# Performance work log

Hardware: AMD Instinct MI355X
Metric: run time of the kernel (lower is better)

## Reference

```python
import jax, jax.numpy as jnp
import numpy as np

E = 256      # feat_dim
H = 4        # num_heads
D = E // H   # head_dim = 64
NC = 7       # num_classes
B = 65536
EPS = 1e-5


def layernorm(x, g, b):
    mu = jnp.mean(x, axis=-1, keepdims=True)
    var = jnp.mean((x - mu) ** 2, axis=-1, keepdims=True)
    return (x - mu) * jax.lax.rsqrt(var + EPS) * g + b


def setup_inputs() -> dict:
    key = jax.random.key(0)
    ks = jax.random.split(key, 16)
    s = 0.02
    return {
        "f_swin":   jax.random.normal(ks[0], (B, E), jnp.float32),
        "f_maxvit": jax.random.normal(ks[1], (B, E), jnp.float32),
        "f_focal":  jax.random.normal(ks[2], (B, E), jnp.float32),
        # MultiheadAttention params (torch packs q,k,v into in_proj)
        "in_proj_w": jax.random.normal(ks[3], (3 * E, E), jnp.float32) * s,
        "in_proj_b": jnp.zeros((3 * E,), jnp.float32),
        "out_w": jax.random.normal(ks[4], (E, E), jnp.float32) * s,
        "out_b": jnp.zeros((E,), jnp.float32),
        # fusion LayerNorm
        "ln1_g": jnp.ones((E,), jnp.float32),
        "ln1_b": jnp.zeros((E,), jnp.float32),
        # gate: Linear(3E, 3)
        "gate_w": jax.random.normal(ks[5], (3, 3 * E), jnp.float32) * s,
        "gate_b": jnp.zeros((3,), jnp.float32),
        # deep_head: LN -> Linear(E,256) -> GELU -> Linear(256,128) -> GELU -> Linear(128,7)
        "ln2_g": jnp.ones((E,), jnp.float32),
        "ln2_b": jnp.zeros((E,), jnp.float32),
        "w1": jax.random.normal(ks[6], (256, E), jnp.float32) * s,
        "b1": jnp.zeros((256,), jnp.float32),
        "w2": jax.random.normal(ks[7], (128, 256), jnp.float32) * s,
        "b2": jnp.zeros((128,), jnp.float32),
        "w3": jax.random.normal(ks[8], (NC, 128), jnp.float32) * s,
        "b3": jnp.zeros((NC,), jnp.float32),
    }


def reference(f_swin, f_maxvit, f_focal, in_proj_w, in_proj_b, out_w, out_b,
              ln1_g, ln1_b, gate_w, gate_b, ln2_g, ln2_b,
              w1, b1, w2, b2, w3, b3):
    # --- AttentionFusionModule ---
    stacked = jnp.stack([f_swin, f_maxvit, f_focal], axis=1)  # [B,3,E]
    qkv = stacked @ in_proj_w.T + in_proj_b                   # [B,3,3E]
    q, k, v = jnp.split(qkv, 3, axis=-1)
    # [B,3,E] -> [B,H,3,D]
    def to_heads(t):
        return t.reshape(t.shape[0], 3, H, D).transpose(0, 2, 1, 3)
    qh, kh, vh = to_heads(q), to_heads(k), to_heads(v)
    scores = jnp.einsum('bhqd,bhkd->bhqk', qh, kh) / jnp.sqrt(jnp.float32(D))
    attn = jax.nn.softmax(scores, axis=-1)
    ctx = jnp.einsum('bhqk,bhkd->bhqd', attn, vh)             # [B,H,3,D]
    ctx = ctx.transpose(0, 2, 1, 3).reshape(-1, 3, E)         # [B,3,E]
    att_out = ctx @ out_w.T + out_b
    x = layernorm(att_out + stacked, ln1_g, ln1_b)            # [B,3,E]
    concat = jnp.concatenate([f_swin, f_maxvit, f_focal], axis=-1)  # [B,3E]
    weights = jax.nn.softmax(concat @ gate_w.T + gate_b, axis=-1)   # [B,3]
    fused = jnp.einsum('bse,bs->be', x, weights)              # [B,E]
    # --- deep_head (Dropout inactive at inference; exact GELU as in torch) ---
    h = layernorm(fused, ln2_g, ln2_b)
    h = jax.nn.gelu(h @ w1.T + b1, approximate=False)
    h = jax.nn.gelu(h @ w2.T + b2, approximate=False)
    logits = h @ w3.T + b3
    return logits, fused
```

## Files before the change

kernel.cpp:

```cpp
#include <hip/hip_runtime.h>
#include <math.h>


#define E   256
#define NC  7
#define BM  16
#define TOK 48
#define NT  256
#define BS  264

typedef unsigned short u16;
typedef unsigned int   u32;
typedef __attribute__((ext_vector_type(8))) short  short8;
typedef __attribute__((ext_vector_type(4))) float  f32x4;

#define O_IPW 0
#define O_OW  196608
#define O_GW  262144
#define O_W1  264448
#define O_W2  329984
#define CVT_TOTAL 362752

__device__ __forceinline__ float bf2f(u32 u) { return __uint_as_float(u << 16); }
__device__ __forceinline__ u16 f2bf(float f) {
    u32 u = __float_as_uint(f);
    return (u16)((u + 0x7fffu + ((u >> 16) & 1u)) >> 16);
}

__global__ void cvt_weights(const float* __restrict__ ipw, const float* __restrict__ ow,
                            const float* __restrict__ gw,  const float* __restrict__ w1,
                            const float* __restrict__ w2,  u16* __restrict__ ws) {
    int i4 = (blockIdx.x * 256 + threadIdx.x) * 4;
    if (i4 >= CVT_TOTAL) return;
    const float* src; int off;
    if      (i4 < O_OW)  { src = ipw; off = i4; }
    else if (i4 < O_GW)  { src = ow;  off = i4 - O_OW; }
    else if (i4 < O_W1)  { src = gw;  off = i4 - O_GW; }
    else if (i4 < O_W2)  { src = w1;  off = i4 - O_W1; }
    else                 { src = w2;  off = i4 - O_W2; }
    float4 v = *(const float4*)(src + off);
    ushort4 o;
    o.x = f2bf(v.x); o.y = f2bf(v.y); o.z = f2bf(v.z); o.w = f2bf(v.w);
    *(ushort4*)(ws + i4) = o;
}

template<int NTW>
__device__ __forceinline__ void issue_b(const u16* __restrict__ bW, int rowBase, int lane,
                                        short8 (&b)[8][NTW]) {
    const int l16 = lane & 15, quad = lane >> 4;
    #pragma unroll
    for (int ks = 0; ks < 8; ++ks)
        #pragma unroll
        for (int j = 0; j < NTW; ++j)
            b[ks][j] = *(const short8*)(bW + (size_t)(rowBase + j * 16 + l16) * 256 + ks * 32 + quad * 8);
}

template<int MT, int NTW>
__device__ __forceinline__ void consume_gemm(const u16* aLds, int aRow0, int lane,
                                             const short8 (&b)[8][NTW], f32x4 (&acc)[MT][NTW]) {
    const int l16 = lane & 15, quad = lane >> 4;
    #pragma unroll
    for (int m = 0; m < MT; ++m)
        #pragma unroll
        for (int j = 0; j < NTW; ++j) acc[m][j] = (f32x4){0.f, 0.f, 0.f, 0.f};
    #pragma unroll
    for (int ks = 0; ks < 8; ++ks) {
        short8 a[MT];
        #pragma unroll
        for (int m = 0; m < MT; ++m)
            a[m] = *(const short8*)(aLds + (size_t)(aRow0 + m * 16 + l16) * BS + ks * 32 + quad * 8);
        #pragma unroll
        for (int j = 0; j < NTW; ++j)
            #pragma unroll
            for (int m = 0; m < MT; ++m)
                acc[m][j] = __builtin_amdgcn_mfma_f32_16x16x32_bf16(a[m], b[ks][j], acc[m][j], 0, 0, 0);
    }
}

__global__ __launch_bounds__(NT, 2)
void dhc_mfma_kernel(
    const float* __restrict__ f0, const float* __restrict__ f1, const float* __restrict__ f2,
    const float* __restrict__ ipb, const float* __restrict__ ob,
    const float* __restrict__ ln1g, const float* __restrict__ ln1b,
    const float* __restrict__ gb,
    const float* __restrict__ ln2g, const float* __restrict__ ln2b,
    const float* __restrict__ b1, const float* __restrict__ b2,
    const float* __restrict__ w3, const float* __restrict__ b3,
    const u16* __restrict__ ws, float* __restrict__ d_out, int nrows)
{
    __shared__ __align__(16) u16 s_x[TOK * BS];
    __shared__ __align__(16) u16 s_buf[TOK * BS];
    __shared__ __align__(16) float s_small[576];
    #define S_ATTN(r,h,q) s_small[((r) * 4 + (h)) * 9 + (q)]
    float* s_mu    = s_small;
    float* s_rstd  = s_small + 48;
    float* s_mu2   = s_small + 96;
    float* s_rstd2 = s_small + 112;

    const int tid  = threadIdx.x;
    const int wid  = tid >> 6, lane = tid & 63;
    const int l16  = lane & 15, quad = lane >> 4;
    const long long row0 = (long long)blockIdx.x * BM;
    const size_t fused_base = (size_t)nrows * NC;

    auto pad_slot = [&](int i) -> float* {
        return (float*)(s_buf + (i >> 2) * BS + 256) + (i & 3);
    };

    const u16* ipw_b = ws + O_IPW;
    const u16* ow_b  = ws + O_OW;
    const u16* gw_b  = ws + O_GW;
    const u16* w1_b  = ws + O_W1;
    const u16* w2_b  = ws + O_W2;

    short8 bq[8][4];
    short8 b5[8][2];

    const int rb0 = (wid < 2) ? (64 * wid) : (256 + 64 * (wid - 2));
    issue_b<4>(ipw_b, rb0, lane, bq);

    #pragma unroll
    for (int it = 0; it < 12; ++it) {
        int id = it * NT + tid;
        int t  = id >> 6;
        int c4 = (id & 63) * 4;
        int s  = t >> 4, r = t & 15;
        float4 v = {0.f, 0.f, 0.f, 0.f};
        if (row0 + r < nrows) {
            const float* src = (s == 0 ? f0 : (s == 1 ? f1 : f2));
            v = *(const float4*)(src + (size_t)(row0 + r) * E + c4);
        }
        ushort4 o;
        o.x = f2bf(v.x); o.y = f2bf(v.y); o.z = f2bf(v.z); o.w = f2bf(v.w);
        *(ushort4*)(s_x + t * BS + c4) = o;
    }
    __syncthreads();

    for (int p = 0; p < 2; ++p) {
        const int rb = rb0 + 128 * p;
        f32x4 acc[3][4];
        consume_gemm<3, 4>(s_x, 0, lane, bq, acc);
        issue_b<4>(ipw_b, (p == 0) ? (rb0 + 128) : (512 + 64 * wid), lane, bq);
        #pragma unroll
        for (int j = 0; j < 4; ++j) {
            int n = wid * 64 + j * 16 + l16;
            float bias = ipb[rb + j * 16 + l16];
            #pragma unroll
            for (int m = 0; m < 3; ++m)
                #pragma unroll
                for (int rr = 0; rr < 4; ++rr) {
                    int tok = m * 16 + quad * 4 + rr;
                    s_buf[tok * BS + n] = f2bf(acc[m][j][rr] + bias);
                }
        }
        __syncthreads();
        if (tid < 96) {
            int r = tid / 6, rem = tid % 6;
            int hh = rem / 3, i = rem % 3;
            int h = 2 * p + hh;
            float d0a = 0.f, d0b = 0.f, d1a = 0.f, d1b = 0.f, d2a = 0.f, d2b = 0.f;
            const u16* qrow = s_buf + (i * 16 + r) * BS + hh * 64;
            const u16* k0 = s_buf + (0 * 16 + r) * BS + 128 + hh * 64;
            const u16* k1 = s_buf + (1 * 16 + r) * BS + 128 + hh * 64;
            const u16* k2 = s_buf + (2 * 16 + r) * BS + 128 + hh * 64;
            for (int d8 = 0; d8 < 8; ++d8) {
                short8 qv = *(const short8*)(qrow + d8 * 8);
                short8 a0 = *(const short8*)(k0 + d8 * 8);
                short8 a1 = *(const short8*)(k1 + d8 * 8);
                short8 a2 = *(const short8*)(k2 + d8 * 8);
                #pragma unroll
                for (int e = 0; e < 4; ++e) {
                    float qa = bf2f((u32)(u16)qv[e]);
                    float qb = bf2f((u32)(u16)qv[e + 4]);
                    d0a += qa * bf2f((u32)(u16)a0[e]); d0b += qb * bf2f((u32)(u16)a0[e + 4]);
                    d1a += qa * bf2f((u32)(u16)a1[e]); d1b += qb * bf2f((u32)(u16)a1[e + 4]);
                    d2a += qa * bf2f((u32)(u16)a2[e]); d2b += qb * bf2f((u32)(u16)a2[e + 4]);
                }
            }
            float d0 = (d0a + d0b) * 0.125f, d1 = (d1a + d1b) * 0.125f, d2 = (d2a + d2b) * 0.125f;
            float mx = fmaxf(d0, fmaxf(d1, d2));
            float e0 = __expf(d0 - mx), e1 = __expf(d1 - mx), e2 = __expf(d2 - mx);
            float inv = 1.f / (e0 + e1 + e2);
            S_ATTN(r, h, i * 3 + 0) = e0 * inv;
            S_ATTN(r, h, i * 3 + 1) = e1 * inv;
            S_ATTN(r, h, i * 3 + 2) = e2 * inv;
        } else if (p == 0 && tid < 240) {
            int idx = tid - 96;
            int r = idx / 9, rem = idx % 9;
            int g = rem / 3, s = rem % 3;
            const u16* xp = s_x + (s * 16 + r) * BS;
            const u16* wp = gw_b + g * 768 + s * 256;
            float a0 = 0.f, a1 = 0.f, a2 = 0.f, a3 = 0.f;
            for (int c8 = 0; c8 < 8; ++c8) {
                #pragma unroll
                for (int q4 = 0; q4 < 4; ++q4) {
                    short8 xv = *(const short8*)(xp + (c8 * 4 + q4) * 8);
                    short8 wv = *(const short8*)(wp + (c8 * 4 + q4) * 8);
                    float t = 0.f;
                    #pragma unroll
                    for (int e = 0; e < 8; ++e)
                        t += bf2f((u32)(u16)xv[e]) * bf2f((u32)(u16)wv[e]);
                    if      (q4 == 0) a0 += t;
                    else if (q4 == 1) a1 += t;
                    else if (q4 == 2) a2 += t;
                    else              a3 += t;
                }
            }
            *pad_slot(idx) = (a0 + a1) + (a2 + a3);
        } else if (p == 1 && tid < 112) {
            int r = tid - 96;
            float l[3];
            #pragma unroll
            for (int g = 0; g < 3; ++g)
                l[g] = gb[g] + *pad_slot(r * 9 + g * 3 + 0)
                             + *pad_slot(r * 9 + g * 3 + 1)
                             + *pad_slot(r * 9 + g * 3 + 2);
            float mx = fmaxf(l[0], fmaxf(l[1], l[2]));
            float e0 = __expf(l[0] - mx), e1 = __expf(l[1] - mx), e2 = __expf(l[2] - mx);
            float inv = 1.f / (e0 + e1 + e2);
            *pad_slot(144 + r * 3 + 0) = e0 * inv;
            *pad_slot(144 + r * 3 + 1) = e1 * inv;
            *pad_slot(144 + r * 3 + 2) = e2 * inv;
        }
        __syncthreads();
    }

    {
        const int rb = 512 + 64 * wid;
        f32x4 acc[3][4];
        consume_gemm<3, 4>(s_x, 0, lane, bq, acc);
        issue_b<4>(ow_b, 64 * wid, lane, bq);
        #pragma unroll
        for (int j = 0; j < 4; ++j) {
            int n = wid * 64 + j * 16 + l16;
            float bias = ipb[rb + j * 16 + l16];
            #pragma unroll
            for (int m = 0; m < 3; ++m)
                #pragma unroll
                for (int rr = 0; rr < 4; ++rr) {
                    int tok = m * 16 + quad * 4 + rr;
                    s_buf[tok * BS + n] = f2bf(acc[m][j][rr] + bias);
                }
        }
    }
    __syncthreads();

    {
        int r = tid >> 4;
        int cb = (tid & 15) * 16;
        int h = cb >> 6;
        float a[9];
        #pragma unroll
        for (int q2 = 0; q2 < 9; ++q2) a[q2] = S_ATTN(r, h, q2);
        #pragma unroll
        for (int cc = 0; cc < 16; ++cc) {
            int c = cb + cc;
            float v0 = bf2f((u32)s_buf[(0 * 16 + r) * BS + c]);
            float v1 = bf2f((u32)s_buf[(1 * 16 + r) * BS + c]);
            float v2 = bf2f((u32)s_buf[(2 * 16 + r) * BS + c]);
            float c0 = a[0] * v0 + a[1] * v1 + a[2] * v2;
            float c1 = a[3] * v0 + a[4] * v1 + a[5] * v2;
            float c2 = a[6] * v0 + a[7] * v1 + a[8] * v2;
            s_buf[(0 * 16 + r) * BS + c] = f2bf(c0);
            s_buf[(1 * 16 + r) * BS + c] = f2bf(c1);
            s_buf[(2 * 16 + r) * BS + c] = f2bf(c2);
        }
    }
    __syncthreads();

    {
        const int rb = 64 * wid;
        f32x4 acc[3][4];
        consume_gemm<3, 4>(s_buf, 0, lane, bq, acc);
        issue_b<4>(w1_b, 64 * wid, lane, bq);
        #pragma unroll
        for (int j = 0; j < 4; ++j) {
            int n = rb + j * 16 + l16;
            float bias = ob[n];
            #pragma unroll
            for (int m = 0; m < 3; ++m)
                #pragma unroll
                for (int rr = 0; rr < 4; ++rr) {
                    int tok = m * 16 + quad * 4 + rr;
                    acc[m][j][rr] += bias + bf2f((u32)s_x[tok * BS + n]);
                }
        }
        __syncthreads();
        #pragma unroll
        for (int j = 0; j < 4; ++j) {
            int n = rb + j * 16 + l16;
            #pragma unroll
            for (int m = 0; m < 3; ++m)
                #pragma unroll
                for (int rr = 0; rr < 4; ++rr) {
                    int tok = m * 16 + quad * 4 + rr;
                    s_buf[tok * BS + n] = f2bf(acc[m][j][rr]);
                }
        }
    }
    __syncthreads();

    if (tid < 192) {
        int r = tid >> 2, j = tid & 3;
        const u16* xp = s_buf + r * BS + j * 64;
        float s0 = 0.f, s1 = 0.f, q0 = 0.f, q1 = 0.f;
        #pragma unroll
        for (int c8 = 0; c8 < 8; ++c8) {
            short8 v = *(const short8*)(xp + c8 * 8);
            #pragma unroll
            for (int e = 0; e < 4; ++e) {
                float xa = bf2f((u32)(u16)v[e]);
                float xb = bf2f((u32)(u16)v[e + 4]);
                s0 += xa; q0 += xa * xa;
                s1 += xb; q1 += xb * xb;
            }
        }
        float sum = s0 + s1, sq = q0 + q1;
        sum += __shfl_xor(sum, 1); sq += __shfl_xor(sq, 1);
        sum += __shfl_xor(sum, 2); sq += __shfl_xor(sq, 2);
        if (j == 0) {
            float mu = sum * (1.f / 256.f);
            float var = sq * (1.f / 256.f) - mu * mu;
            s_mu[r] = mu;
            s_rstd[r] = rsqrtf(var + 1e-5f);
        }
    }
    __syncthreads();
    {
        float g = ln1g[tid], b = ln1b[tid];
        #pragma unroll 4
        for (int t = 0; t < TOK; ++t) {
            float x = bf2f((u32)s_buf[t * BS + tid]);
            s_buf[t * BS + tid] = f2bf((x - s_mu[t]) * s_rstd[t] * g + b);
        }
    }
    __syncthreads();

    {
        int c = tid;
        float* outF = d_out + fused_base;
        #pragma unroll 4
        for (int r = 0; r < BM; ++r) {
            float w0 = *pad_slot(144 + r * 3 + 0);
            float w1v = *pad_slot(144 + r * 3 + 1);
            float w2v = *pad_slot(144 + r * 3 + 2);
            float f = w0  * bf2f((u32)s_buf[(0 * 16 + r) * BS + c])
                    + w1v * bf2f((u32)s_buf[(1 * 16 + r) * BS + c])
                    + w2v * bf2f((u32)s_buf[(2 * 16 + r) * BS + c]);
            if (row0 + r < nrows) outF[(size_t)(row0 + r) * E + c] = f;
            s_buf[r * BS + c] = f2bf(f);
        }
    }
    __syncthreads();

    {
        int r = tid >> 4, j = tid & 15;
        const u16* fp = s_buf + r * BS + j * 16;
        float sum = 0.f, sq = 0.f;
        #pragma unroll
        for (int c8 = 0; c8 < 2; ++c8) {
            short8 v = *(const short8*)(fp + c8 * 8);
            #pragma unroll
            for (int e = 0; e < 8; ++e) {
                float x = bf2f((u32)(u16)v[e]);
                sum += x; sq += x * x;
            }
        }
        sum += __shfl_xor(sum, 1); sq += __shfl_xor(sq, 1);
        sum += __shfl_xor(sum, 2); sq += __shfl_xor(sq, 2);
        sum += __shfl_xor(sum, 4); sq += __shfl_xor(sq, 4);
        sum += __shfl_xor(sum, 8); sq += __shfl_xor(sq, 8);
        if (j == 0) {
            float mu = sum * (1.f / 256.f);
            float var = sq * (1.f / 256.f) - mu * mu;
            s_mu2[r] = mu;
            s_rstd2[r] = rsqrtf(var + 1e-5f);
        }
    }
    __syncthreads();
    {
        float g = ln2g[tid], b = ln2b[tid];
        #pragma unroll
        for (int r = 0; r < BM; ++r) {
            float x = bf2f((u32)s_buf[r * BS + tid]);
            s_buf[r * BS + tid] = f2bf((x - s_mu2[r]) * s_rstd2[r] * g + b);
        }
    }
    __syncthreads();

    {
        const int rb = 64 * wid;
        f32x4 acc[1][4];
        consume_gemm<1, 4>(s_buf, 0, lane, bq, acc);
        issue_b<2>(w2_b, 32 * wid, lane, b5);
        __syncthreads();
        #pragma unroll
        for (int j = 0; j < 4; ++j) {
            int n = rb + j * 16 + l16;
            float bias = b1[n];
            #pragma unroll
            for (int rr = 0; rr < 4; ++rr) {
                int r = quad * 4 + rr;
                float x = acc[0][j][rr] + bias;
                float hgelu = 0.5f * x * (1.f + erff(x * 0.70710678118654752f));
                s_buf[(16 + r) * BS + n] = f2bf(hgelu);
            }
        }
    }
    __syncthreads();

    {
        const int rb = 32 * wid;
        f32x4 acc[1][2];
        consume_gemm<1, 2>(s_buf, 16, lane, b5, acc);
        __syncthreads();
        #pragma unroll
        for (int j = 0; j < 2; ++j) {
            int n = rb + j * 16 + l16;
            float bias = b2[n];
            #pragma unroll
            for (int rr = 0; rr < 4; ++rr) {
                int r = quad * 4 + rr;
                float x = acc[0][j][rr] + bias;
                float hgelu = 0.5f * x * (1.f + erff(x * 0.70710678118654752f));
                s_buf[(32 + r) * BS + n] = f2bf(hgelu);
            }
        }
    }
    __syncthreads();

    if (tid < BM * NC) {
        int r = tid / NC, n = tid % NC;
        const float* wr = w3 + n * 128;
        const u16* hp = s_buf + (32 + r) * BS;
        float a0 = 0.f, a1 = 0.f, a2 = 0.f, a3 = 0.f;
        #pragma unroll
        for (int q8 = 0; q8 < 8; ++q8) {
            #pragma unroll
            for (int q4 = 0; q4 < 4; ++q4) {
                int k4 = q8 * 4 + q4;
                float4 w = *(const float4*)(wr + k4 * 4);
                float t = bf2f((u32)hp[k4 * 4 + 0]) * w.x
                        + bf2f((u32)hp[k4 * 4 + 1]) * w.y
                        + bf2f((u32)hp[k4 * 4 + 2]) * w.z
                        + bf2f((u32)hp[k4 * 4 + 3]) * w.w;
                if      (q4 == 0) a0 += t;
                else if (q4 == 1) a1 += t;
                else if (q4 == 2) a2 += t;
                else              a3 += t;
            }
        }
        float acc = b3[n] + (a0 + a1) + (a2 + a3);
        if (row0 + r < nrows) d_out[(size_t)(row0 + r) * NC + n] = acc;
    }
}

extern "C" void kernel_launch(void* const* d_in, const int* in_sizes, int n_in,
                              void* d_out, int out_size, void* d_ws, size_t ws_size,
                              hipStream_t stream) {
    (void)n_in; (void)ws_size; (void)out_size;
    const int nrows = in_sizes[0] / E;
    u16* ws = (u16*)d_ws;
    cvt_weights<<<(CVT_TOTAL / 4 + 255) / 256, 256, 0, stream>>>(
        (const float*)d_in[3], (const float*)d_in[5], (const float*)d_in[9],
        (const float*)d_in[13], (const float*)d_in[15], ws);
    const int nblocks = (nrows + BM - 1) / BM;
    dhc_mfma_kernel<<<nblocks, NT, 0, stream>>>(
        (const float*)d_in[0], (const float*)d_in[1], (const float*)d_in[2],
        (const float*)d_in[4], (const float*)d_in[6],
        (const float*)d_in[7], (const float*)d_in[8],
        (const float*)d_in[10],
        (const float*)d_in[11], (const float*)d_in[12],
        (const float*)d_in[14], (const float*)d_in[16],
        (const float*)d_in[17], (const float*)d_in[18],
        ws, (float*)d_out, nrows);
}
```

Baseline: 722.6 us.

## Restructure attention stage per head, shrink LDS and drop register-prefetched weights

```diff
diff --git a/kernel.cpp b/kernel.cpp
--- a/kernel.cpp
+++ b/kernel.cpp
@@ -7,7 +7,8 @@
 #define BM  16
 #define TOK 48
 #define NT  256
-#define BS  264
+#define BSX 264
+#define BSB 136
 
 typedef unsigned short u16;
 typedef unsigned int   u32;
@@ -44,36 +45,30 @@
     *(ushort4*)(ws + i4) = o;
 }
 
-template<int NTW>
-__device__ __forceinline__ void issue_b(const u16* __restrict__ bW, int rowBase, int lane,
-                                        short8 (&b)[8][NTW]) {
+template<int MT, int NTW, int KSN, int AS, bool ZERO>
+__device__ __forceinline__ void gemm_tile(const u16* aLds, int aRow0, int aCol0,
+                                          const u16* __restrict__ bW, int rowBase, int bCol0,
+                                          int lane, f32x4 (&acc)[MT][NTW]) {
     const int l16 = lane & 15, quad = lane >> 4;
+    if (ZERO) {
+        #pragma unroll
+        for (int m = 0; m < MT; ++m)
+            #pragma unroll
+            for (int j = 0; j < NTW; ++j) acc[m][j] = (f32x4){0.f, 0.f, 0.f, 0.f};
+    }
     #pragma unroll
-    for (int ks = 0; ks < 8; ++ks)
-        #pragma unroll
-        for (int j = 0; j < NTW; ++j)
-            b[ks][j] = *(const short8*)(bW + (size_t)(rowBase + j * 16 + l16) * 256 + ks * 32 + quad * 8);
-}
-
-template<int MT, int NTW>
-__device__ __forceinline__ void consume_gemm(const u16* aLds, int aRow0, int lane,
-                                             const short8 (&b)[8][NTW], f32x4 (&acc)[MT][NTW]) {
-    const int l16 = lane & 15, quad = lane >> 4;
-    #pragma unroll
-    for (int m = 0; m < MT; ++m)
-        #pragma unroll
-        for (int j = 0; j < NTW; ++j) acc[m][j] = (f32x4){0.f, 0.f, 0.f, 0.f};
-    #pragma unroll
-    for (int ks = 0; ks < 8; ++ks) {
+    for (int ks = 0; ks < KSN; ++ks) {
         short8 a[MT];
         #pragma unroll
         for (int m = 0; m < MT; ++m)
-            a[m] = *(const short8*)(aLds + (size_t)(aRow0 + m * 16 + l16) * BS + ks * 32 + quad * 8);
-        #pragma unroll
-        for (int j = 0; j < NTW; ++j)
+            a[m] = *(const short8*)(aLds + (size_t)(aRow0 + m * 16 + l16) * AS + aCol0 + ks * 32 + quad * 8);
+        #pragma unroll
+        for (int j = 0; j < NTW; ++j) {
+            short8 b = *(const short8*)(bW + (size_t)(rowBase + j * 16 + l16) * 256 + bCol0 + ks * 32 + quad * 8);
             #pragma unroll
             for (int m = 0; m < MT; ++m)
-                acc[m][j] = __builtin_amdgcn_mfma_f32_16x16x32_bf16(a[m], b[ks][j], acc[m][j], 0, 0, 0);
+                acc[m][j] = __builtin_amdgcn_mfma_f32_16x16x32_bf16(a[m], b, acc[m][j], 0, 0, 0);
+        }
     }
 }
 
@@ -88,14 +83,10 @@
     const float* __restrict__ w3, const float* __restrict__ b3,
     const u16* __restrict__ ws, float* __restrict__ d_out, int nrows)
 {
-    __shared__ __align__(16) u16 s_x[TOK * BS];
-    __shared__ __align__(16) u16 s_buf[TOK * BS];
-    __shared__ __align__(16) float s_small[576];
+    __shared__ __align__(16) u16 s_x[TOK * BSX];
+    __shared__ __align__(16) u16 s_buf[TOK * BSB];
+    __shared__ __align__(16) float s_small[640];
     #define S_ATTN(r,h,q) s_small[((r) * 4 + (h)) * 9 + (q)]
-    float* s_mu    = s_small;
-    float* s_rstd  = s_small + 48;
-    float* s_mu2   = s_small + 96;
-    float* s_rstd2 = s_small + 112;
 
     const int tid  = threadIdx.x;
     const int wid  = tid >> 6, lane = tid & 63;
@@ -103,8 +94,8 @@
     const long long row0 = (long long)blockIdx.x * BM;
     const size_t fused_base = (size_t)nrows * NC;
 
-    auto pad_slot = [&](int i) -> float* {
-        return (float*)(s_buf + (i >> 2) * BS + 256) + (i & 3);
+    auto gp_slot = [&](int i) -> float* {
+        return (float*)(s_x + (i >> 2) * BSX + 256) + (i & 3);
     };
 
     const u16* ipw_b = ws + O_IPW;
@@ -112,12 +103,6 @@
     const u16* gw_b  = ws + O_GW;
     const u16* w1_b  = ws + O_W1;
     const u16* w2_b  = ws + O_W2;
-
-    short8 bq[8][4];
-    short8 b5[8][2];
-
-    const int rb0 = (wid < 2) ? (64 * wid) : (256 + 64 * (wid - 2));
-    issue_b<4>(ipw_b, rb0, lane, bq);
 
     #pragma unroll
     for (int it = 0; it < 12; ++it) {
@@ -132,63 +117,52 @@
         }
         ushort4 o;
         o.x = f2bf(v.x); o.y = f2bf(v.y); o.z = f2bf(v.z); o.w = f2bf(v.w);
-        *(ushort4*)(s_x + t * BS + c4) = o;
-    }
-    __syncthreads();
-
-    for (int p = 0; p < 2; ++p) {
-        const int rb = rb0 + 128 * p;
-        f32x4 acc[3][4];
-        consume_gemm<3, 4>(s_x, 0, lane, bq, acc);
-        issue_b<4>(ipw_b, (p == 0) ? (rb0 + 128) : (512 + 64 * wid), lane, bq);
-        #pragma unroll
-        for (int j = 0; j < 4; ++j) {
-            int n = wid * 64 + j * 16 + l16;
-            float bias = ipb[rb + j * 16 + l16];
-            #pragma unroll
-            for (int m = 0; m < 3; ++m)
-                #pragma unroll
-                for (int rr = 0; rr < 4; ++rr) {
-                    int tok = m * 16 + quad * 4 + rr;
-                    s_buf[tok * BS + n] = f2bf(acc[m][j][rr] + bias);
-                }
-        }
-        __syncthreads();
-        if (tid < 96) {
-            int r = tid / 6, rem = tid % 6;
-            int hh = rem / 3, i = rem % 3;
-            int h = 2 * p + hh;
-            float d0a = 0.f, d0b = 0.f, d1a = 0.f, d1b = 0.f, d2a = 0.f, d2b = 0.f;
-            const u16* qrow = s_buf + (i * 16 + r) * BS + hh * 64;
-            const u16* k0 = s_buf + (0 * 16 + r) * BS + 128 + hh * 64;
-            const u16* k1 = s_buf + (1 * 16 + r) * BS + 128 + hh * 64;
-            const u16* k2 = s_buf + (2 * 16 + r) * BS + 128 + hh * 64;
-            for (int d8 = 0; d8 < 8; ++d8) {
-                short8 qv = *(const short8*)(qrow + d8 * 8);
-                short8 a0 = *(const short8*)(k0 + d8 * 8);
-                short8 a1 = *(const short8*)(k1 + d8 * 8);
-                short8 a2 = *(const short8*)(k2 + d8 * 8);
-                #pragma unroll
-                for (int e = 0; e < 4; ++e) {
-                    float qa = bf2f((u32)(u16)qv[e]);
-                    float qb = bf2f((u32)(u16)qv[e + 4]);
-                    d0a += qa * bf2f((u32)(u16)a0[e]); d0b += qb * bf2f((u32)(u16)a0[e + 4]);
-                    d1a += qa * bf2f((u32)(u16)a1[e]); d1b += qb * bf2f((u32)(u16)a1[e + 4]);
-                    d2a += qa * bf2f((u32)(u16)a2[e]); d2b += qb * bf2f((u32)(u16)a2[e + 4]);
-                }
-            }
-            float d0 = (d0a + d0b) * 0.125f, d1 = (d1a + d1b) * 0.125f, d2 = (d2a + d2b) * 0.125f;
-            float mx = fmaxf(d0, fmaxf(d1, d2));
-            float e0 = __expf(d0 - mx), e1 = __expf(d1 - mx), e2 = __expf(d2 - mx);
-            float inv = 1.f / (e0 + e1 + e2);
-            S_ATTN(r, h, i * 3 + 0) = e0 * inv;
-            S_ATTN(r, h, i * 3 + 1) = e1 * inv;
-            S_ATTN(r, h, i * 3 + 2) = e2 * inv;
-        } else if (p == 0 && tid < 240) {
-            int idx = tid - 96;
+        *(ushort4*)(s_x + t * BSX + c4) = o;
+    }
+    __syncthreads();
+
+    auto softmax_head = [&](int hh) {
+        int i = tid >> 4, r = tid & 15;
+        const u16* qrow = s_buf + (i * 16 + r) * BSB;
+        const u16* k0 = s_buf + (0 * 16 + r) * BSB + 64;
+        const u16* k1 = s_buf + (1 * 16 + r) * BSB + 64;
+        const u16* k2 = s_buf + (2 * 16 + r) * BSB + 64;
+        float d0a = 0.f, d0b = 0.f, d1a = 0.f, d1b = 0.f, d2a = 0.f, d2b = 0.f;
+        #pragma unroll
+        for (int d8 = 0; d8 < 8; ++d8) {
+            short8 qv = *(const short8*)(qrow + d8 * 8);
+            short8 a0 = *(const short8*)(k0 + d8 * 8);
+            short8 a1 = *(const short8*)(k1 + d8 * 8);
+            short8 a2 = *(const short8*)(k2 + d8 * 8);
+            #pragma unroll
+            for (int e = 0; e < 4; ++e) {
+                float qa = bf2f((u32)(u16)qv[e]);
+                float qb = bf2f((u32)(u16)qv[e + 4]);
+                d0a += qa * bf2f((u32)(u16)a0[e]); d0b += qb * bf2f((u32)(u16)a0[e + 4]);
+                d1a += qa * bf2f((u32)(u16)a1[e]); d1b += qb * bf2f((u32)(u16)a1[e + 4]);
+                d2a += qa * bf2f((u32)(u16)a2[e]); d2b += qb * bf2f((u32)(u16)a2[e + 4]);
+            }
+        }
+        float d0 = (d0a + d0b) * 0.125f, d1 = (d1a + d1b) * 0.125f, d2 = (d2a + d2b) * 0.125f;
+        float mx = fmaxf(d0, fmaxf(d1, d2));
+        float e0 = __expf(d0 - mx), e1 = __expf(d1 - mx), e2 = __expf(d2 - mx);
+        float inv = 1.f / (e0 + e1 + e2);
+        S_ATTN(r, hh, i * 3 + 0) = e0 * inv;
+        S_ATTN(r, hh, i * 3 + 1) = e1 * inv;
+        S_ATTN(r, hh, i * 3 + 2) = e2 * inv;
+    };
+
+    for (int h = 0; h < 4; ++h) {
+        const int rbh = (wid < 2) ? (64 * h + 32 * wid)
+                                  : (256 + 64 * h + 32 * (wid - 2));
+        f32x4 acc[3][2];
+        gemm_tile<3, 2, 8, BSX, true>(s_x, 0, 0, ipw_b, rbh, 0, lane, acc);
+        if (h > 0 && tid < 48) softmax_head(h - 1);
+        if (h == 0 && tid >= 48 && tid < 192) {
+            int idx = tid - 48;
             int r = idx / 9, rem = idx % 9;
             int g = rem / 3, s = rem % 3;
-            const u16* xp = s_x + (s * 16 + r) * BS;
+            const u16* xp = s_x + (s * 16 + r) * BSX;
             const u16* wp = gw_b + g * 768 + s * 256;
             float a0 = 0.f, a1 = 0.f, a2 = 0.f, a3 = 0.f;
             for (int c8 = 0; c8 < 8; ++c8) {
@@ -206,103 +180,109 @@
                     else              a3 += t;
                 }
             }
-            *pad_slot(idx) = (a0 + a1) + (a2 + a3);
-        } else if (p == 1 && tid < 112) {
-            int r = tid - 96;
+            *gp_slot(idx) = (a0 + a1) + (a2 + a3);
+        }
+        if (h == 1 && tid >= 48 && tid < 64) {
+            int r = tid - 48;
             float l[3];
             #pragma unroll
             for (int g = 0; g < 3; ++g)
-                l[g] = gb[g] + *pad_slot(r * 9 + g * 3 + 0)
-                             + *pad_slot(r * 9 + g * 3 + 1)
-                             + *pad_slot(r * 9 + g * 3 + 2);
+                l[g] = gb[g] + *gp_slot(r * 9 + g * 3 + 0)
+                             + *gp_slot(r * 9 + g * 3 + 1)
+                             + *gp_slot(r * 9 + g * 3 + 2);
             float mx = fmaxf(l[0], fmaxf(l[1], l[2]));
             float e0 = __expf(l[0] - mx), e1 = __expf(l[1] - mx), e2 = __expf(l[2] - mx);
             float inv = 1.f / (e0 + e1 + e2);
-            *pad_slot(144 + r * 3 + 0) = e0 * inv;
-            *pad_slot(144 + r * 3 + 1) = e1 * inv;
-            *pad_slot(144 + r * 3 + 2) = e2 * inv;
-        }
-        __syncthreads();
-    }
-
-    {
-        const int rb = 512 + 64 * wid;
-        f32x4 acc[3][4];
-        consume_gemm<3, 4>(s_x, 0, lane, bq, acc);
-        issue_b<4>(ow_b, 64 * wid, lane, bq);
-        #pragma unroll
-        for (int j = 0; j < 4; ++j) {
-            int n = wid * 64 + j * 16 + l16;
-            float bias = ipb[rb + j * 16 + l16];
+            s_small[576 + r * 3 + 0] = e0 * inv;
+            s_small[576 + r * 3 + 1] = e1 * inv;
+            s_small[576 + r * 3 + 2] = e2 * inv;
+        }
+        __syncthreads();
+        const int nl = (wid < 2) ? (32 * wid) : (64 + 32 * (wid - 2));
+        #pragma unroll
+        for (int j = 0; j < 2; ++j) {
+            int nn = nl + j * 16 + l16;
+            float bias = ipb[rbh + j * 16 + l16];
             #pragma unroll
             for (int m = 0; m < 3; ++m)
                 #pragma unroll
                 for (int rr = 0; rr < 4; ++rr) {
                     int tok = m * 16 + quad * 4 + rr;
-                    s_buf[tok * BS + n] = f2bf(acc[m][j][rr] + bias);
+                    s_buf[tok * BSB + nn] = f2bf(acc[m][j][rr] + bias);
                 }
         }
-    }
-    __syncthreads();
-
-    {
-        int r = tid >> 4;
-        int cb = (tid & 15) * 16;
-        int h = cb >> 6;
-        float a[9];
-        #pragma unroll
-        for (int q2 = 0; q2 < 9; ++q2) a[q2] = S_ATTN(r, h, q2);
-        #pragma unroll
-        for (int cc = 0; cc < 16; ++cc) {
-            int c = cb + cc;
-            float v0 = bf2f((u32)s_buf[(0 * 16 + r) * BS + c]);
-            float v1 = bf2f((u32)s_buf[(1 * 16 + r) * BS + c]);
-            float v2 = bf2f((u32)s_buf[(2 * 16 + r) * BS + c]);
-            float c0 = a[0] * v0 + a[1] * v1 + a[2] * v2;
-            float c1 = a[3] * v0 + a[4] * v1 + a[5] * v2;
-            float c2 = a[6] * v0 + a[7] * v1 + a[8] * v2;
-            s_buf[(0 * 16 + r) * BS + c] = f2bf(c0);
-            s_buf[(1 * 16 + r) * BS + c] = f2bf(c1);
-            s_buf[(2 * 16 + r) * BS + c] = f2bf(c2);
-        }
-    }
-    __syncthreads();
-
-    {
-        const int rb = 64 * wid;
-        f32x4 acc[3][4];
-        consume_gemm<3, 4>(s_buf, 0, lane, bq, acc);
-        issue_b<4>(w1_b, 64 * wid, lane, bq);
-        #pragma unroll
-        for (int j = 0; j < 4; ++j) {
-            int n = rb + j * 16 + l16;
-            float bias = ob[n];
-            #pragma unroll
-            for (int m = 0; m < 3; ++m)
+        __syncthreads();
+    }
+
+    f32x4 acc3[3][4];
+
+    for (int hv = 0; hv < 2; ++hv) {
+        {
+            const int rb = 512 + 128 * hv + 32 * wid;
+            f32x4 acc[3][2];
+            gemm_tile<3, 2, 8, BSX, true>(s_x, 0, 0, ipw_b, rb, 0, lane, acc);
+            if (hv == 0 && tid < 48) softmax_head(3);
+            __syncthreads();
+            #pragma unroll
+            for (int j = 0; j < 2; ++j) {
+                int nn = 32 * wid + j * 16 + l16;
+                float bias = ipb[rb + j * 16 + l16];
                 #pragma unroll
-                for (int rr = 0; rr < 4; ++rr) {
-                    int tok = m * 16 + quad * 4 + rr;
-                    acc[m][j][rr] += bias + bf2f((u32)s_x[tok * BS + n]);
-                }
-        }
-        __syncthreads();
-        #pragma unroll
-        for (int j = 0; j < 4; ++j) {
-            int n = rb + j * 16 + l16;
-            #pragma unroll
-            for (int m = 0; m < 3; ++m)
+                for (int m = 0; m < 3; ++m)
+                    #pragma unroll
+                    for (int rr = 0; rr < 4; ++rr) {
+                        int tok = m * 16 + quad * 4 + rr;
+                        s_buf[tok * BSB + nn] = f2bf(acc[m][j][rr] + bias);
+                    }
+            }
+        }
+        __syncthreads();
+        {
+            int r  = tid >> 4;
+            int cb = (tid & 15) * 8;
+            int h  = 2 * hv + (cb >> 6);
+            float a[9];
+            #pragma unroll
+            for (int q2 = 0; q2 < 9; ++q2) a[q2] = S_ATTN(r, h, q2);
+            #pragma unroll
+            for (int cc = 0; cc < 8; ++cc) {
+                int c = cb + cc;
+                float v0 = bf2f((u32)s_buf[(0 * 16 + r) * BSB + c]);
+                float v1 = bf2f((u32)s_buf[(1 * 16 + r) * BSB + c]);
+                float v2 = bf2f((u32)s_buf[(2 * 16 + r) * BSB + c]);
+                float c0 = a[0] * v0 + a[1] * v1 + a[2] * v2;
+                float c1 = a[3] * v0 + a[4] * v1 + a[5] * v2;
+                float c2 = a[6] * v0 + a[7] * v1 + a[8] * v2;
+                s_buf[(0 * 16 + r) * BSB + c] = f2bf(c0);
+                s_buf[(1 * 16 + r) * BSB + c] = f2bf(c1);
+                s_buf[(2 * 16 + r) * BSB + c] = f2bf(c2);
+            }
+        }
+        __syncthreads();
+        if (hv == 0) {
+            gemm_tile<3, 4, 4, BSB, true >(s_buf, 0, 0, ow_b, 64 * wid, 0,   lane, acc3);
+        } else {
+            gemm_tile<3, 4, 4, BSB, false>(s_buf, 0, 0, ow_b, 64 * wid, 128, lane, acc3);
+            #pragma unroll
+            for (int j = 0; j < 4; ++j) {
+                int n = 64 * wid + j * 16 + l16;
+                float bias = ob[n];
                 #pragma unroll
-                for (int rr = 0; rr < 4; ++rr) {
-                    int tok = m * 16 + quad * 4 + rr;
-                    s_buf[tok * BS + n] = f2bf(acc[m][j][rr]);
-                }
-        }
-    }
-    __syncthreads();
+                for (int m = 0; m < 3; ++m)
+                    #pragma unroll
+                    for (int rr = 0; rr < 4; ++rr) {
+                        int tok = m * 16 + quad * 4 + rr;
+                        float v = acc3[m][j][rr] + bias + bf2f((u32)s_x[tok * BSX + n]);
+                        s_x[tok * BSX + n] = f2bf(v);
+                    }
+            }
+        }
+        __syncthreads();
+    }
 
     if (tid < 192) {
         int r = tid >> 2, j = tid & 3;
-        const u16* xp = s_buf + r * BS + j * 64;
+        const u16* xp = s_x + r * BSX + j * 64;
         float s0 = 0.f, s1 = 0.f, q0 = 0.f, q1 = 0.f;
         #pragma unroll
         for (int c8 = 0; c8 < 8; ++c8) {
@@ -321,8 +301,8 @@
         if (j == 0) {
             float mu = sum * (1.f / 256.f);
             float var = sq * (1.f / 256.f) - mu * mu;
-            s_mu[r] = mu;
-            s_rstd[r] = rsqrtf(var + 1e-5f);
+            s_small[r] = mu;
+            s_small[48 + r] = rsqrtf(var + 1e-5f);
         }
     }
     __syncthreads();
@@ -330,8 +310,8 @@
         float g = ln1g[tid], b = ln1b[tid];
         #pragma unroll 4
         for (int t = 0; t < TOK; ++t) {
-            float x = bf2f((u32)s_buf[t * BS + tid]);
-            s_buf[t * BS + tid] = f2bf((x - s_mu[t]) * s_rstd[t] * g + b);
+            float x = bf2f((u32)s_x[t * BSX + tid]);
+            s_x[t * BSX + tid] = f2bf((x - s_small[t]) * s_small[48 + t] * g + b);
         }
     }
     __syncthreads();
@@ -341,21 +321,21 @@
         float* outF = d_out + fused_base;
         #pragma unroll 4
         for (int r = 0; r < BM; ++r) {
-            float w0 = *pad_slot(144 + r * 3 + 0);
-            float w1v = *pad_slot(144 + r * 3 + 1);
-            float w2v = *pad_slot(144 + r * 3 + 2);
-            float f = w0  * bf2f((u32)s_buf[(0 * 16 + r) * BS + c])
-                    + w1v * bf2f((u32)s_buf[(1 * 16 + r) * BS + c])
-                    + w2v * bf2f((u32)s_buf[(2 * 16 + r) * BS + c]);
+            float w0 = s_small[576 + r * 3 + 0];
+            float w1v = s_small[576 + r * 3 + 1];
+            float w2v = s_small[576 + r * 3 + 2];
+            float f = w0  * bf2f((u32)s_x[(0 * 16 + r) * BSX + c])
+                    + w1v * bf2f((u32)s_x[(1 * 16 + r) * BSX + c])
+                    + w2v * bf2f((u32)s_x[(2 * 16 + r) * BSX + c]);
             if (row0 + r < nrows) outF[(size_t)(row0 + r) * E + c] = f;
-            s_buf[r * BS + c] = f2bf(f);
+            s_buf[r * BSX + c] = f2bf(f);
         }
     }
     __syncthreads();
 
     {
         int r = tid >> 4, j = tid & 15;
-        const u16* fp = s_buf + r * BS + j * 16;
+        const u16* fp = s_buf + r * BSX + j * 16;
         float sum = 0.f, sq = 0.f;
         #pragma unroll
         for (int c8 = 0; c8 < 2; ++c8) {
@@ -373,8 +353,8 @@
         if (j == 0) {
             float mu = sum * (1.f / 256.f);
             float var = sq * (1.f / 256.f) - mu * mu;
-            s_mu2[r] = mu;
-            s_rstd2[r] = rsqrtf(var + 1e-5f);
+            s_small[96 + r] = mu;
+            s_small[112 + r] = rsqrtf(var + 1e-5f);
         }
     }
     __syncthreads();
@@ -382,48 +362,45 @@
         float g = ln2g[tid], b = ln2b[tid];
         #pragma unroll
         for (int r = 0; r < BM; ++r) {
-            float x = bf2f((u32)s_buf[r * BS + tid]);
-            s_buf[r * BS + tid] = f2bf((x - s_mu2[r]) * s_rstd2[r] * g + b);
-        }
-    }
-    __syncthreads();
-
-    {
-        const int rb = 64 * wid;
+            float x = bf2f((u32)s_buf[r * BSX + tid]);
+            s_buf[r * BSX + tid] = f2bf((x - s_small[96 + r]) * s_small[112 + r] * g + b);
+        }
+    }
+    __syncthreads();
+
+    {
         f32x4 acc[1][4];
-        consume_gemm<1, 4>(s_buf, 0, lane, bq, acc);
-        issue_b<2>(w2_b, 32 * wid, lane, b5);
+        gemm_tile<1, 4, 8, BSX, true>(s_buf, 0, 0, w1_b, 64 * wid, 0, lane, acc);
         __syncthreads();
         #pragma unroll
         for (int j = 0; j < 4; ++j) {
-            int n = rb + j * 16 + l16;
+            int n = 64 * wid + j * 16 + l16;
             float bias = b1[n];
             #pragma unroll
             for (int rr = 0; rr < 4; ++rr) {
                 int r = quad * 4 + rr;
                 float x = acc[0][j][rr] + bias;
                 float hgelu = 0.5f * x * (1.f + erff(x * 0.70710678118654752f));
-                s_buf[(16 + r) * BS + n] = f2bf(hgelu);
-            }
-        }
-    }
-    __syncthreads();
-
-    {
-        const int rb = 32 * wid;
+                s_buf[r * BSX + n] = f2bf(hgelu);
+            }
+        }
+    }
+    __syncthreads();
+
+    {
         f32x4 acc[1][2];
-        consume_gemm<1, 2>(s_buf, 16, lane, b5, acc);
+        gemm_tile<1, 2, 8, BSX, true>(s_buf, 0, 0, w2_b, 32 * wid, 0, lane, acc);
         __syncthreads();
         #pragma unroll
         for (int j = 0; j < 2; ++j) {
-            int n = rb + j * 16 + l16;
+            int n = 32 * wid + j * 16 + l16;
             float bias = b2[n];
             #pragma unroll
             for (int rr = 0; rr < 4; ++rr) {
                 int r = quad * 4 + rr;
                 float x = acc[0][j][rr] + bias;
                 float hgelu = 0.5f * x * (1.f + erff(x * 0.70710678118654752f));
-                s_buf[(32 + r) * BS + n] = f2bf(hgelu);
+                s_buf[r * BSB + n] = f2bf(hgelu);
             }
         }
     }
@@ -432,7 +409,7 @@
     if (tid < BM * NC) {
         int r = tid / NC, n = tid % NC;
         const float* wr = w3 + n * 128;
-        const u16* hp = s_buf + (32 + r) * BS;
+        const u16* hp = s_buf + r * BSB;
         float a0 = 0.f, a1 = 0.f, a2 = 0.f, a3 = 0.f;
         #pragma unroll
         for (int q8 = 0; q8 < 8; ++q8) {
```

Result: no change. 716.5 us (-0.8%).
